# Kernel optimization log

Measured on AMD Instinct MI355X. Metric: run time of the kernel, lower is better.

## Reference

```python
import jax, jax.numpy as jnp
import numpy as np

S, B, D_MODEL, H = 2048, 2, 1024, 16
DH = D_MODEL // H
SCALE = 1.0 / np.sqrt(DH)
NEG_INF = jnp.float32(-1e30)


def setup_inputs() -> dict:
    key = jax.random.key(0)
    ks = jax.random.split(key, 12)
    std = 1.0 / np.sqrt(D_MODEL)
    inp = {
        "query": jax.random.normal(ks[0], (S, B, D_MODEL), jnp.float32),
        "key": jax.random.normal(ks[1], (S, B, D_MODEL), jnp.float32),
        "value": jax.random.normal(ks[2], (S, B, D_MODEL), jnp.float32),
        # causal mask, shape (seq_q, seq_k, 1) per prepare_mask asserts
        "mask": jnp.tril(jnp.ones((S, S), dtype=bool))[:, :, None],
        # params stored (in, out) for x @ W
        "Wq": jax.random.normal(ks[3], (D_MODEL, H * DH), jnp.float32) * std,
        "bq": jnp.zeros((H * DH,), jnp.float32),
        "Wk": jax.random.normal(ks[4], (D_MODEL, H * DH), jnp.float32) * std,
        "bk": jnp.zeros((H * DH,), jnp.float32),
        "Wv": jax.random.normal(ks[5], (D_MODEL, H * DH), jnp.float32) * std,
        "bv": jnp.zeros((H * DH,), jnp.float32),
        "Wo": jax.random.normal(ks[6], (D_MODEL, D_MODEL), jnp.float32) * std,
        "bo": jnp.zeros((D_MODEL,), jnp.float32),
    }
    return inp


def reference(query, key, value, mask, Wq, bq, Wk, bk, Wv, bv, Wo, bo):
    seq_len, batch, _ = query.shape
    # project and split heads: (S, B, H, DH)
    q = (query @ Wq + bq).reshape(seq_len, batch, H, DH)
    k = (key @ Wk + bk).reshape(key.shape[0], batch, H, DH)
    v = (value @ Wv + bv).reshape(value.shape[0], batch, H, DH)
    # scores: (seq_q, batch, heads, seq_k)
    scores = jnp.einsum("ibhd,jbhd->ibhj", q, k) * SCALE
    # mask (seq_q, seq_k, batch_or_1) -> broadcast to (seq_q, batch, 1, seq_k)
    m = jnp.transpose(mask, (0, 2, 1))[:, :, None, :]
    scores = jnp.where(m, scores, NEG_INF)
    attn = jax.nn.softmax(scores, axis=-1)  # dropout_prob=0.0 (eval)
    x = jnp.einsum("ibhj,jbhd->ibhd", attn, v)
    x = x.reshape(seq_len, batch, H * DH)
    return x @ Wo + bo
```

## Files before the change

kernel.cpp:

```cpp
#include <hip/hip_runtime.h>
#include <hip/hip_bf16.h>
#include <cstdint>

#define S_LEN 2048
#define BATCH 2
#define DM    1024
#define NH    16
#define DH    64

typedef short s8v __attribute__((ext_vector_type(8)));
typedef float f4v __attribute__((ext_vector_type(4)));
typedef unsigned int u32x2 __attribute__((ext_vector_type(2)));

__device__ __forceinline__ ushort f2bf(float x) {
  union { float f; uint32_t u; } v; v.f = x;
  uint32_t r = v.u + 0x7fffu + ((v.u >> 16) & 1u);
  return (ushort)(r >> 16);
}
__device__ __forceinline__ float bf2f(ushort u) {
  union { uint32_t u; float f; } v; v.u = (uint32_t)u << 16; return v.f;
}
__device__ __forceinline__ uint32_t fbits(float x) {
  union { float f; uint32_t u; } v; v.f = x; return v.u;
}
__device__ __forceinline__ uint32_t bfrnd(uint32_t u) {
  return u + 0x7fffu + ((u >> 16) & 1u);
}
__device__ __forceinline__ uint32_t packbf(uint32_t flo, uint32_t fhi) {
  return __builtin_amdgcn_perm(bfrnd(fhi), bfrnd(flo), 0x07060302u);
}
__device__ __forceinline__ uint32_t packbf_tr(float lo, float hi) {
  return __builtin_amdgcn_perm(fbits(hi), fbits(lo), 0x07060302u);
}

typedef __attribute__((address_space(1))) const void gas_void;
typedef __attribute__((address_space(3))) void las_void;
__device__ __forceinline__ void gld16(void* l, const void* g) {
  __builtin_amdgcn_global_load_lds((gas_void*)(uintptr_t)g,
                                   (las_void*)(uintptr_t)l, 16, 0, 0);
}

__global__ __launch_bounds__(256)
void prep(const float* W0, const float* W1, const float* W2, const float* W3,
          ushort* T0, ushort* T1, ushort* T2, ushort* T3,
          const float* X0, const float* X1, const float* X2,
          ushort* O0, ushort* O1, ushort* O2) {
  const int z = blockIdx.z;
  if (z < 4) {
    if (blockIdx.x >= 1024) return;
    const float* W = z == 0 ? W0 : z == 1 ? W1 : z == 2 ? W2 : W3;
    ushort*      T = z == 0 ? T0 : z == 1 ? T1 : z == 2 ? T2 : T3;
    __shared__ ushort tile[32][33];
    const int n0 = (blockIdx.x & 31) * 32, k0 = (blockIdx.x >> 5) * 32;
    const int tx = threadIdx.x & 31, ty = threadIdx.x >> 5;
    #pragma unroll
    for (int r = ty; r < 32; r += 8)
      tile[r][tx] = f2bf(W[(size_t)(k0 + r) * DM + n0 + tx]);
    __syncthreads();
    #pragma unroll
    for (int r = ty; r < 32; r += 8)
      T[(size_t)(n0 + r) * DM + k0 + tx] = tile[tx][r];
  } else {
    const float* X = z == 4 ? X0 : z == 5 ? X1 : X2;
    ushort*      O = z == 4 ? O0 : z == 5 ? O1 : O2;
    const size_t i = ((size_t)blockIdx.x * 256 + threadIdx.x) * 4;
    const float4 v = *(const float4*)(X + i);
    ushort4 h;
    h.x = f2bf(v.x); h.y = f2bf(v.y); h.z = f2bf(v.z); h.w = f2bf(v.w);
    *(ushort4*)(O + i) = h;
  }
}

__global__ __launch_bounds__(512, 2)
void gemm_qkv(const ushort* __restrict__ Xq, const ushort* __restrict__ Xk,
              const ushort* __restrict__ Xv,
              const ushort* __restrict__ Wqt, const ushort* __restrict__ Wkt,
              const ushort* __restrict__ Wvt,
              const float* __restrict__ bq, const float* __restrict__ bk,
              const float* __restrict__ bv,
              ushort* __restrict__ Qh, ushort* __restrict__ Kh,
              ushort* __restrict__ Vt) {
  const int z = blockIdx.z;
  const ushort* A    = z == 0 ? Xq  : z == 1 ? Xk  : Xv;
  const ushort* Bt   = z == 0 ? Wqt : z == 1 ? Wkt : Wvt;
  const float*  bias = z == 0 ? bq  : z == 1 ? bk  : bv;

  __shared__ __align__(16) ushort lds[65536];

  const int tid = threadIdx.x, lane = tid & 63, w = tid >> 6;
  const int wm = w >> 2, wn = w & 3;
  const int lrow = lane & 15, quad = lane >> 4;
  const int m0 = blockIdx.x * 256, n0 = blockIdx.y * 256;

  const int tr = tid >> 2;
  const int swz = ((tid & 3) ^ ((tid >> 3) & 3)) * 8;
  const ushort* gA0 = A  + (size_t)(m0 + tr) * DM + swz;
  const ushort* gA1 = A  + (size_t)(m0 + 128 + tr) * DM + swz;
  const ushort* gB0 = Bt + (size_t)(n0 + tr) * DM + swz;
  const ushort* gB1 = Bt + (size_t)(n0 + 128 + tr) * DM + swz;
  const int dA0 = w * 512, dA1 = 4096 + w * 512;
  const int dB0 = 8192 + w * 512, dB1 = 12288 + w * 512;

  const int fr = (lrow >> 1) & 3;
  int pa[8], pb[4];
  #pragma unroll
  for (int i = 0; i < 8; i++)
    pa[i] = (wm * 128 + i * 16 + lrow) * 32 + ((quad ^ fr) * 8);
  #pragma unroll
  for (int j = 0; j < 4; j++)
    pb[j] = 8192 + (wn * 64 + j * 16 + lrow) * 32 + ((quad ^ fr) * 8);

  f4v acc[8][4];
  #pragma unroll
  for (int i = 0; i < 8; i++)
    #pragma unroll
    for (int j = 0; j < 4; j++)
      acc[i][j] = f4v{0.f, 0.f, 0.f, 0.f};

  #pragma unroll
  for (int t = 0; t < 3; t++) {
    const int bb = t * 16384, ko = t * 32;
    gld16(&lds[bb + dA0], gA0 + ko);
    gld16(&lds[bb + dA1], gA1 + ko);
    gld16(&lds[bb + dB0], gB0 + ko);
    gld16(&lds[bb + dB1], gB1 + ko);
  }
  asm volatile("s_waitcnt vmcnt(8)" ::: "memory");
  __builtin_amdgcn_s_barrier();

  for (int t = 0; t < 32; t++) {
    const int bb = (t & 3) * 16384;
    const bool st = t < 29;
    const int sbb = ((t + 3) & 3) * 16384;
    const int ko = (t + 3) * 32;
    s8v af[4], bf[4];
    #pragma unroll
    for (int i = 0; i < 4; i++) af[i] = *(const s8v*)&lds[bb + pa[i]];
    #pragma unroll
    for (int j = 0; j < 4; j++) bf[j] = *(const s8v*)&lds[bb + pb[j]];
    if (st) { gld16(&lds[sbb + dA0], gA0 + ko); gld16(&lds[sbb + dA1], gA1 + ko); }
    __builtin_amdgcn_s_barrier();
    __builtin_amdgcn_s_setprio(1);
    #pragma unroll
    for (int i = 0; i < 4; i++)
      #pragma unroll
      for (int j = 0; j < 4; j++)
        acc[i][j] = __builtin_amdgcn_mfma_f32_16x16x32_bf16(af[i], bf[j], acc[i][j], 0, 0, 0);
    __builtin_amdgcn_s_setprio(0);
    __builtin_amdgcn_s_barrier();
    #pragma unroll
    for (int i = 0; i < 4; i++) af[i] = *(const s8v*)&lds[bb + pa[4 + i]];
    if (st) { gld16(&lds[sbb + dB0], gB0 + ko); gld16(&lds[sbb + dB1], gB1 + ko); }
    __builtin_amdgcn_s_barrier();
    __builtin_amdgcn_s_setprio(1);
    #pragma unroll
    for (int i = 0; i < 4; i++)
      #pragma unroll
      for (int j = 0; j < 4; j++)
        acc[4 + i][j] = __builtin_amdgcn_mfma_f32_16x16x32_bf16(af[i], bf[j], acc[4 + i][j], 0, 0, 0);
    __builtin_amdgcn_s_setprio(0);
    if (t < 29)       asm volatile("s_waitcnt vmcnt(8)" ::: "memory");
    else if (t == 29) asm volatile("s_waitcnt vmcnt(4)" ::: "memory");
    else if (t == 30) asm volatile("s_waitcnt vmcnt(0)" ::: "memory");
    __builtin_amdgcn_s_barrier();
  }

  if (z <= 1) {
    ushort* O = (z == 0) ? Qh : Kh;
    #pragma unroll
    for (int i = 0; i < 8; i++)
      #pragma unroll
      for (int j = 0; j < 4; j++) {
        const int n = n0 + wn * 64 + j * 16 + lrow;
        const float bval = bias[n];
        const int h = n >> 6, d = n & 63;
        const int mb = m0 + wm * 128 + i * 16 + quad * 4;
        #pragma unroll
        for (int r = 0; r < 4; r++) {
          const int m = mb + r;
          O[((size_t)((m & 1) * NH + h) * S_LEN + (m >> 1)) * DH + d] = f2bf(acc[i][j][r] + bval);
        }
      }
  } else {
    ushort* tw = lds + w * 5120;
    const int h = (n0 + wn * 64) >> 6;
    const int s0b = (m0 + wm * 128) >> 1;
    #pragma unroll
    for (int mh = 0; mh < 2; mh++) {
      #pragma unroll
      for (int i = 0; i < 4; i++)
        #pragma unroll
        for (int j = 0; j < 4; j++) {
          const int d_l = j * 16 + lrow;
          const float bval = bias[n0 + wn * 64 + d_l];
          const f4v a = acc[mh * 4 + i][j];
          const int sbase = i * 8 + quad * 2;
          const uint32_t p0 = packbf(fbits(a[0] + bval), fbits(a[2] + bval));
          const uint32_t p1 = packbf(fbits(a[1] + bval), fbits(a[3] + bval));
          *(uint32_t*)&tw[d_l * 40 + sbase]        = p0;
          *(uint32_t*)&tw[2560 + d_l * 40 + sbase] = p1;
        }
      const int s0 = s0b + mh * 32;
      #pragma unroll
      for (int b = 0; b < 2; b++)
        #pragma unroll
        for (int p = 0; p < 4; p++) {
          const int d_l = p * 16 + (lane >> 2);
          const int c   = lane & 3;
          const s8v v = *(const s8v*)&tw[b * 2560 + d_l * 40 + c * 8];
          *(s8v*)&Vt[((size_t)(b * NH + h) * DH + d_l) * S_LEN + s0 + c * 8] = v;
        }
      if (mh == 0) __builtin_amdgcn_s_barrier();
    }
  }
}

__global__ __launch_bounds__(256)
void attn(const ushort* __restrict__ Qh, const ushort* __restrict__ Kh,
          const ushort* __restrict__ Vt, ushort* __restrict__ X,
          ushort* __restrict__ Opart, float* __restrict__ lpart) {
  __shared__ __align__(16) ushort lds[2 * 8192];

  const int tid = threadIdx.x, lane = tid & 63, w = tid >> 6;
  const int lrow = lane & 15, quad = lane >> 4;
  const int bh = blockIdx.x;
  const int slot = blockIdx.y;
  int qt, part, nparts;
  if (slot < 18)      { qt = 15 - slot / 3;        part = slot % 3;        nparts = 3; }
  else if (slot < 30) { qt = 9  - (slot - 18) / 2; part = (slot - 18) % 2; nparts = 2; }
  else                { qt = 33 - slot;            part = 0;               nparts = 1; }
  const int nj  = 2 * qt + 2;
  const int jlo = part * nj / nparts;
  const int jhi = (part + 1) * nj / nparts;
  const int iw  = qt * 128 + w * 32;

  const int srow = lane >> 3;
  const int scol = ((lane & 7) ^ srow) * 8;
  const ushort* gK0 = Kh + ((size_t)bh * S_LEN + 2 * w * 8 + srow) * DH + scol;
  const ushort* gK1 = gK0 + 8 * DH;
  const ushort* gV0 = Vt + ((size_t)bh * DH + 2 * w * 8 + srow) * S_LEN + scol;
  const ushort* gV1 = gV0 + 8 * S_LEN;
  const int lK0 = 2 * w * 512, lK1 = lK0 + 512;
  const int lV0 = 4096 + 2 * w * 512, lV1 = lV0 + 512;

  s8v aq[2][2];
  #pragma unroll
  for (int is = 0; is < 2; is++)
    #pragma unroll
    for (int kk = 0; kk < 2; kk++)
      aq[is][kk] = *(const s8v*)(Qh + ((size_t)bh * S_LEN + iw + is * 16 + lrow) * DH +
                                 kk * 32 + quad * 8);

  const int f8 = lrow & 7;
  int pk[4][2], pv[4][2];
  #pragma unroll
  for (int s4 = 0; s4 < 4; s4++)
    #pragma unroll
    for (int kk = 0; kk < 2; kk++) {
      pk[s4][kk] = (s4 * 16 + lrow) * 64 + (((kk * 4 + quad) ^ f8) * 8);
      pv[s4][kk] = 4096 + (s4 * 16 + lrow) * 64 + (((kk * 4 + quad) ^ f8) * 8);
    }

  f4v o[2][4];
  f4v lacc[2];
  #pragma unroll
  for (int is = 0; is < 2; is++) {
    lacc[is] = f4v{0.f, 0.f, 0.f, 0.f};
    #pragma unroll
    for (int d4 = 0; d4 < 4; d4++) o[is][d4] = f4v{0.f, 0.f, 0.f, 0.f};
  }
  const s8v vones = {0x3F80, 0x3F80, 0x3F80, 0x3F80, 0x3F80, 0x3F80, 0x3F80, 0x3F80};

  {
    const int b0 = (jlo & 1) * 8192;
    const size_t j0 = (size_t)jlo * 64;
    gld16(&lds[b0 + lK0], gK0 + j0 * DH);
    gld16(&lds[b0 + lK1], gK1 + j0 * DH);
    gld16(&lds[b0 + lV0], gV0 + j0);
    gld16(&lds[b0 + lV1], gV1 + j0);
  }

  for (int jt = jlo; jt < jhi; jt++) {
    const int j0 = jt * 64;
    asm volatile("s_waitcnt vmcnt(0)" ::: "memory");
    __builtin_amdgcn_s_barrier();
    const int cur = (jt & 1) * 8192;
    if (jt + 1 < jhi) {
      const int nb = ((jt + 1) & 1) * 8192;
      const size_t jn = (size_t)(jt + 1) * 64;
      gld16(&lds[nb + lK0], gK0 + jn * DH);
      gld16(&lds[nb + lK1], gK1 + jn * DH);
      gld16(&lds[nb + lV0], gV0 + jn);
      gld16(&lds[nb + lV1], gV1 + jn);
    }
    if (j0 > iw + 31) continue;

    f4v sc[2][4];
    #pragma unroll
    for (int is = 0; is < 2; is++)
      #pragma unroll
      for (int s4 = 0; s4 < 4; s4++) sc[is][s4] = f4v{0.f, 0.f, 0.f, 0.f};
    __builtin_amdgcn_s_setprio(1);
    #pragma unroll
    for (int s4 = 0; s4 < 4; s4++) {
      const s8v k0f = *(const s8v*)&lds[cur + pk[s4][0]];
      const s8v k1f = *(const s8v*)&lds[cur + pk[s4][1]];
      sc[0][s4] = __builtin_amdgcn_mfma_f32_16x16x32_bf16(k0f, aq[0][0], sc[0][s4], 0, 0, 0);
      sc[1][s4] = __builtin_amdgcn_mfma_f32_16x16x32_bf16(k0f, aq[1][0], sc[1][s4], 0, 0, 0);
      sc[0][s4] = __builtin_amdgcn_mfma_f32_16x16x32_bf16(k1f, aq[0][1], sc[0][s4], 0, 0, 0);
      sc[1][s4] = __builtin_amdgcn_mfma_f32_16x16x32_bf16(k1f, aq[1][1], sc[1][s4], 0, 0, 0);
    }
    __builtin_amdgcn_s_setprio(0);

    const bool needmask = (j0 + 63) > iw;
    const float C = 0.18033688011112042f;
    uint32_t sw[2][4][2];
    #pragma unroll
    for (int is = 0; is < 2; is++) {
      const int ig = iw + is * 16 + lrow;
      #pragma unroll
      for (int s4 = 0; s4 < 4; s4++) {
        float e0 = __builtin_amdgcn_exp2f(sc[is][s4][0] * C);
        float e1 = __builtin_amdgcn_exp2f(sc[is][s4][1] * C);
        float e2 = __builtin_amdgcn_exp2f(sc[is][s4][2] * C);
        float e3 = __builtin_amdgcn_exp2f(sc[is][s4][3] * C);
        if (needmask) {
          const int jb = j0 + s4 * 16 + quad * 4;
          e0 = (jb + 0 > ig) ? 0.f : e0;
          e1 = (jb + 1 > ig) ? 0.f : e1;
          e2 = (jb + 2 > ig) ? 0.f : e2;
          e3 = (jb + 3 > ig) ? 0.f : e3;
        }
        sw[is][s4][0] = packbf_tr(e0, e1);
        sw[is][s4][1] = packbf_tr(e2, e3);
      }
    }

    s8v ap[2][2];
    #pragma unroll
    for (int is = 0; is < 2; is++)
      #pragma unroll
      for (int kt = 0; kt < 2; kt++) {
        const u32x2 a32 = __builtin_amdgcn_permlane32_swap(
            sw[is][2 * kt][0], sw[is][2 * kt + 1][0], false, false);
        const u32x2 a16 = __builtin_amdgcn_permlane16_swap(a32[0], a32[1], false, false);
        const u32x2 b32 = __builtin_amdgcn_permlane32_swap(
            sw[is][2 * kt][1], sw[is][2 * kt + 1][1], false, false);
        const u32x2 b16 = __builtin_amdgcn_permlane16_swap(b32[0], b32[1], false, false);
        union { uint32_t u[4]; s8v v; } cvt;
        cvt.u[0] = a16[0]; cvt.u[1] = b16[0]; cvt.u[2] = a16[1]; cvt.u[3] = b16[1];
        ap[is][kt] = cvt.v;
      }

    __builtin_amdgcn_s_setprio(1);
    #pragma unroll
    for (int d4 = 0; d4 < 4; d4++) {
      const s8v v0 = *(const s8v*)&lds[cur + pv[d4][0]];
      const s8v v1 = *(const s8v*)&lds[cur + pv[d4][1]];
      o[0][d4] = __builtin_amdgcn_mfma_f32_16x16x32_bf16(ap[0][0], v0, o[0][d4], 0, 0, 0);
      o[1][d4] = __builtin_amdgcn_mfma_f32_16x16x32_bf16(ap[1][0], v0, o[1][d4], 0, 0, 0);
      o[0][d4] = __builtin_amdgcn_mfma_f32_16x16x32_bf16(ap[0][1], v1, o[0][d4], 0, 0, 0);
      o[1][d4] = __builtin_amdgcn_mfma_f32_16x16x32_bf16(ap[1][1], v1, o[1][d4], 0, 0, 0);
    }
    lacc[0] = __builtin_amdgcn_mfma_f32_16x16x32_bf16(ap[0][0], vones, lacc[0], 0, 0, 0);
    lacc[0] = __builtin_amdgcn_mfma_f32_16x16x32_bf16(ap[0][1], vones, lacc[0], 0, 0, 0);
    lacc[1] = __builtin_amdgcn_mfma_f32_16x16x32_bf16(ap[1][0], vones, lacc[1], 0, 0, 0);
    lacc[1] = __builtin_amdgcn_mfma_f32_16x16x32_bf16(ap[1][1], vones, lacc[1], 0, 0, 0);
    __builtin_amdgcn_s_setprio(0);
  }

  if (nparts == 1) {
    const int bb = bh >> 4, h = bh & 15;
    #pragma unroll
    for (int is = 0; is < 2; is++)
      #pragma unroll
      for (int r = 0; r < 4; r++) {
        const float inv = 1.0f / lacc[is][r];
        const int sg = iw + is * 16 + quad * 4 + r;
        #pragma unroll
        for (int d4 = 0; d4 < 4; d4++)
          X[((size_t)sg * BATCH + bb) * DM + h * DH + d4 * 16 + lrow] =
              f2bf(o[is][d4][r] * inv);
      }
  } else {
    ushort* Op = Opart + ((size_t)(bh * 30 + slot) * 128 + w * 32) * 64;
    #pragma unroll
    for (int is = 0; is < 2; is++)
      #pragma unroll
      for (int r = 0; r < 4; r++) {
        const int row_l = is * 16 + quad * 4 + r;
        #pragma unroll
        for (int d4 = 0; d4 < 4; d4++)
          Op[row_l * 64 + d4 * 16 + lrow] = f2bf(o[is][d4][r]);
      }
    if (lrow == 0) {
      float* lp = lpart + (size_t)(bh * 30 + slot) * 128 + w * 32;
      #pragma unroll
      for (int is = 0; is < 2; is++)
        #pragma unroll
        for (int r = 0; r < 4; r++)
          lp[is * 16 + quad * 4 + r] = lacc[is][r];
    }
  }
}

__global__ __launch_bounds__(256)
void combine(const ushort* __restrict__ Opart, const float* __restrict__ lpart,
             ushort* __restrict__ X) {
  const uint32_t gid = blockIdx.x * 256 + threadIdx.x;
  const int dv   = gid & 15;
  const int row  = (gid >> 4) & 127;
  const int rest = gid >> 11;
  const int qi   = rest % 12;
  const int bh   = rest / 12;
  const int qt   = 4 + qi;
  int s0, c;
  if (qt >= 10) { s0 = 3 * (15 - qt); c = 3; }
  else          { s0 = 18 + 2 * (9 - qt); c = 2; }

  float a0 = 0.f, a1 = 0.f, a2 = 0.f, a3 = 0.f, l = 0.f;
  #pragma unroll
  for (int p = 0; p < 3; p++) {
    if (p < c) {
      const size_t base = ((size_t)(bh * 30 + s0 + p) * 128 + row);
      const ushort4 v = *(const ushort4*)&Opart[base * 64 + dv * 4];
      a0 += bf2f(v.x); a1 += bf2f(v.y); a2 += bf2f(v.z); a3 += bf2f(v.w);
      l += lpart[base];
    }
  }
  const float inv = 1.0f / l;
  const int qpos = qt * 128 + row;
  const int b = bh >> 4, h = bh & 15;
  ushort4 hv;
  hv.x = f2bf(a0 * inv);
  hv.y = f2bf(a1 * inv);
  hv.z = f2bf(a2 * inv);
  hv.w = f2bf(a3 * inv);
  *(ushort4*)&X[(((size_t)qpos * BATCH + b) * NH + h) * DH + dv * 4] = hv;
}

__global__ __launch_bounds__(256)
void gemm_out(const ushort* __restrict__ A, const ushort* __restrict__ Bt,
              const float* __restrict__ bias, float* __restrict__ C) {
  __shared__ __align__(16) ushort lds[16384];

  const int tid = threadIdx.x, lane = tid & 63, w = tid >> 6;
  const int wr = w >> 1, wc = w & 1;
  const int lrow = lane & 15, quad = lane >> 4;
  const int m0 = blockIdx.x * 128, n0 = blockIdx.y * 128;

  const int sr4 = lane >> 2;
  const int scol = ((lane & 3) ^ (sr4 & 3)) * 8;

  const ushort* gA[2]; const ushort* gB[2];
  int oA[2], oB[2];
  #pragma unroll
  for (int t = 0; t < 2; t++) {
    const int c = 2 * w + t;
    gA[t] = A  + (size_t)(m0 + c * 16 + sr4) * DM + scol;
    oA[t] = c * 512;
    gB[t] = Bt + (size_t)(n0 + c * 16 + sr4) * DM + scol;
    oB[t] = 4096 + c * 512;
  }

  int pa[4], pb[4];
  #pragma unroll
  for (int i = 0; i < 4; i++) {
    pa[i] = (wr * 64 + i * 16 + lrow) * 32 + ((quad ^ (lrow & 3)) * 8);
    pb[i] = 4096 + (wc * 64 + i * 16 + lrow) * 32 + ((quad ^ (lrow & 3)) * 8);
  }

  f4v acc[4][4];
  #pragma unroll
  for (int i = 0; i < 4; i++)
    #pragma unroll
    for (int j = 0; j < 4; j++)
      acc[i][j] = f4v{0.f, 0.f, 0.f, 0.f};

  #pragma unroll
  for (int t = 0; t < 2; t++) {
    gld16(&lds[oA[t]], gA[t]);
    gld16(&lds[oB[t]], gB[t]);
  }

  for (int ks = 0; ks < 32; ks++) {
    __syncthreads();
    const int bo = (ks & 1) * 8192;
    if (ks < 31) {
      const int nb = ((ks + 1) & 1) * 8192;
      const int ko = (ks + 1) * 32;
      #pragma unroll
      for (int t = 0; t < 2; t++) {
        gld16(&lds[nb + oA[t]], gA[t] + ko);
        gld16(&lds[nb + oB[t]], gB[t] + ko);
      }
    }
    s8v af[4], bf[4];
    #pragma unroll
    for (int i = 0; i < 4; i++) af[i] = *(const s8v*)&lds[bo + pa[i]];
    #pragma unroll
    for (int j = 0; j < 4; j++) bf[j] = *(const s8v*)&lds[bo + pb[j]];
    #pragma unroll
    for (int i = 0; i < 4; i++)
      #pragma unroll
      for (int j = 0; j < 4; j++)
        acc[i][j] = __builtin_amdgcn_mfma_f32_16x16x32_bf16(af[i], bf[j], acc[i][j], 0, 0, 0);
  }

  #pragma unroll
  for (int i = 0; i < 4; i++)
    #pragma unroll
    for (int j = 0; j < 4; j++) {
      const int n = n0 + wc * 64 + j * 16 + lrow;
      const float bval = bias[n];
      const int mb = m0 + wr * 64 + i * 16 + quad * 4;
      #pragma unroll
      for (int r = 0; r < 4; r++)
        C[(size_t)(mb + r) * DM + n] = acc[i][j][r] + bval;
    }
}

extern "C" void kernel_launch(void* const* d_in, const int* in_sizes, int n_in,
                              void* d_out, int out_size, void* d_ws, size_t ws_size,
                              hipStream_t stream) {
  const float* query = (const float*)d_in[0];
  const float* key_  = (const float*)d_in[1];
  const float* value = (const float*)d_in[2];
  const float* Wq = (const float*)d_in[4];
  const float* bq = (const float*)d_in[5];
  const float* Wk = (const float*)d_in[6];
  const float* bk = (const float*)d_in[7];
  const float* Wv = (const float*)d_in[8];
  const float* bv = (const float*)d_in[9];
  const float* Wo = (const float*)d_in[10];
  const float* bo = (const float*)d_in[11];

  ushort* Wqt = (ushort*)d_ws;
  ushort* Wkt = Wqt + (size_t)1024 * 1024;
  ushort* Wvt = Wkt + (size_t)1024 * 1024;
  ushort* Wot = Wvt + (size_t)1024 * 1024;
  ushort* Xbq = Wot + (size_t)1024 * 1024;
  ushort* Xbk = Xbq + (size_t)4 * 1024 * 1024;
  ushort* Xbv = Xbk + (size_t)4 * 1024 * 1024;
  ushort* Qh  = Xbv + (size_t)4 * 1024 * 1024;
  ushort* Kh  = Qh  + (size_t)4 * 1024 * 1024;
  ushort* Vt  = Kh  + (size_t)4 * 1024 * 1024;
  ushort* Opart = Xbk;
  float*  lpart = (float*)Wqt;
  ushort* Xa  = Xbq;

  prep<<<dim3(4096, 1, 7), 256, 0, stream>>>(Wq, Wk, Wv, Wo, Wqt, Wkt, Wvt, Wot,
                                             query, key_, value, Xbq, Xbk, Xbv);
  gemm_qkv<<<dim3(16, 4, 3), 512, 0, stream>>>(Xbq, Xbk, Xbv,
                                               Wqt, Wkt, Wvt, bq, bk, bv,
                                               Qh, Kh, Vt);
  attn<<<dim3(32, 34), 256, 0, stream>>>(Qh, Kh, Vt, Xa, Opart, lpart);
  combine<<<3072, 256, 0, stream>>>(Opart, lpart, Xa);
  gemm_out<<<dim3(32, 8), 256, 0, stream>>>(Xa, Wot, bo, (float*)d_out);
}
```

Baseline: 225.9 us.

## Shrink QKV GEMM tiles, triple-buffer attention K/V, 4-stage pipeline for output GEMM

The QKV projection GEMM moves from 256x256 tiles with 512 threads to 128x128 tiles with 256 threads. This gives 768 blocks instead of 192, so the CUs are better filled. The attention kernel goes from double to triple buffering of K/V tiles, so loads are issued two iterations ahead and the wait only drains the older batch. The output GEMM takes on the same 4-stage async LDS pipeline with split barriers and priority hints that the QKV GEMM uses. Smaller tiles lower data reuse per block, and the extra LDS in attention may reduce occupancy.

```diff
diff --git a/kernel.cpp b/kernel.cpp
--- a/kernel.cpp
+++ b/kernel.cpp
@@ -71,7 +71,7 @@
   }
 }
 
-__global__ __launch_bounds__(512, 2)
+__global__ __launch_bounds__(256, 2)
 void gemm_qkv(const ushort* __restrict__ Xq, const ushort* __restrict__ Xk,
               const ushort* __restrict__ Xv,
               const ushort* __restrict__ Wqt, const ushort* __restrict__ Wkt,
@@ -85,79 +85,80 @@
   const ushort* Bt   = z == 0 ? Wqt : z == 1 ? Wkt : Wvt;
   const float*  bias = z == 0 ? bq  : z == 1 ? bk  : bv;
 
-  __shared__ __align__(16) ushort lds[65536];
+  __shared__ __align__(16) ushort lds[32768];
 
   const int tid = threadIdx.x, lane = tid & 63, w = tid >> 6;
-  const int wm = w >> 2, wn = w & 3;
+  const int wm = w >> 1, wn = w & 1;
   const int lrow = lane & 15, quad = lane >> 4;
-  const int m0 = blockIdx.x * 256, n0 = blockIdx.y * 256;
-
-  const int tr = tid >> 2;
-  const int swz = ((tid & 3) ^ ((tid >> 3) & 3)) * 8;
-  const ushort* gA0 = A  + (size_t)(m0 + tr) * DM + swz;
-  const ushort* gA1 = A  + (size_t)(m0 + 128 + tr) * DM + swz;
-  const ushort* gB0 = Bt + (size_t)(n0 + tr) * DM + swz;
-  const ushort* gB1 = Bt + (size_t)(n0 + 128 + tr) * DM + swz;
-  const int dA0 = w * 512, dA1 = 4096 + w * 512;
-  const int dB0 = 8192 + w * 512, dB1 = 12288 + w * 512;
+  const int m0 = blockIdx.x * 128, n0 = blockIdx.y * 128;
+
+  const int sr4 = lane >> 2;
+  const int scol = ((lane & 3) ^ ((lane >> 3) & 3)) * 8;
+  const ushort* gA[2]; const ushort* gB[2];
+  int dA[2], dB[2];
+  #pragma unroll
+  for (int t = 0; t < 2; t++) {
+    const int c = 2 * w + t;
+    gA[t] = A  + (size_t)(m0 + c * 16 + sr4) * DM + scol;
+    dA[t] = c * 512;
+    gB[t] = Bt + (size_t)(n0 + c * 16 + sr4) * DM + scol;
+    dB[t] = 4096 + c * 512;
+  }
 
   const int fr = (lrow >> 1) & 3;
-  int pa[8], pb[4];
-  #pragma unroll
-  for (int i = 0; i < 8; i++)
-    pa[i] = (wm * 128 + i * 16 + lrow) * 32 + ((quad ^ fr) * 8);
-  #pragma unroll
-  for (int j = 0; j < 4; j++)
-    pb[j] = 8192 + (wn * 64 + j * 16 + lrow) * 32 + ((quad ^ fr) * 8);
-
-  f4v acc[8][4];
-  #pragma unroll
-  for (int i = 0; i < 8; i++)
+  int pa[4], pb[4];
+  #pragma unroll
+  for (int i = 0; i < 4; i++) {
+    pa[i] = (wm * 64 + i * 16 + lrow) * 32 + ((quad ^ fr) * 8);
+    pb[i] = 4096 + (wn * 64 + i * 16 + lrow) * 32 + ((quad ^ fr) * 8);
+  }
+
+  f4v acc[4][4];
+  #pragma unroll
+  for (int i = 0; i < 4; i++)
     #pragma unroll
     for (int j = 0; j < 4; j++)
       acc[i][j] = f4v{0.f, 0.f, 0.f, 0.f};
 
   #pragma unroll
   for (int t = 0; t < 3; t++) {
-    const int bb = t * 16384, ko = t * 32;
-    gld16(&lds[bb + dA0], gA0 + ko);
-    gld16(&lds[bb + dA1], gA1 + ko);
-    gld16(&lds[bb + dB0], gB0 + ko);
-    gld16(&lds[bb + dB1], gB1 + ko);
+    const int bb = t * 8192, ko = t * 32;
+    gld16(&lds[bb + dA[0]], gA[0] + ko);
+    gld16(&lds[bb + dA[1]], gA[1] + ko);
+    gld16(&lds[bb + dB[0]], gB[0] + ko);
+    gld16(&lds[bb + dB[1]], gB[1] + ko);
   }
   asm volatile("s_waitcnt vmcnt(8)" ::: "memory");
   __builtin_amdgcn_s_barrier();
 
   for (int t = 0; t < 32; t++) {
-    const int bb = (t & 3) * 16384;
+    const int bb = (t & 3) * 8192;
     const bool st = t < 29;
-    const int sbb = ((t + 3) & 3) * 16384;
+    const int sbb = ((t + 3) & 3) * 8192;
     const int ko = (t + 3) * 32;
     s8v af[4], bf[4];
     #pragma unroll
     for (int i = 0; i < 4; i++) af[i] = *(const s8v*)&lds[bb + pa[i]];
     #pragma unroll
     for (int j = 0; j < 4; j++) bf[j] = *(const s8v*)&lds[bb + pb[j]];
-    if (st) { gld16(&lds[sbb + dA0], gA0 + ko); gld16(&lds[sbb + dA1], gA1 + ko); }
+    if (st) { gld16(&lds[sbb + dA[0]], gA[0] + ko); gld16(&lds[sbb + dA[1]], gA[1] + ko); }
     __builtin_amdgcn_s_barrier();
     __builtin_amdgcn_s_setprio(1);
     #pragma unroll
-    for (int i = 0; i < 4; i++)
+    for (int i = 0; i < 2; i++)
       #pragma unroll
       for (int j = 0; j < 4; j++)
         acc[i][j] = __builtin_amdgcn_mfma_f32_16x16x32_bf16(af[i], bf[j], acc[i][j], 0, 0, 0);
     __builtin_amdgcn_s_setprio(0);
     __builtin_amdgcn_s_barrier();
-    #pragma unroll
-    for (int i = 0; i < 4; i++) af[i] = *(const s8v*)&lds[bb + pa[4 + i]];
-    if (st) { gld16(&lds[sbb + dB0], gB0 + ko); gld16(&lds[sbb + dB1], gB1 + ko); }
+    if (st) { gld16(&lds[sbb + dB[0]], gB[0] + ko); gld16(&lds[sbb + dB[1]], gB[1] + ko); }
     __builtin_amdgcn_s_barrier();
     __builtin_amdgcn_s_setprio(1);
     #pragma unroll
-    for (int i = 0; i < 4; i++)
+    for (int i = 2; i < 4; i++)
       #pragma unroll
       for (int j = 0; j < 4; j++)
-        acc[4 + i][j] = __builtin_amdgcn_mfma_f32_16x16x32_bf16(af[i], bf[j], acc[4 + i][j], 0, 0, 0);
+        acc[i][j] = __builtin_amdgcn_mfma_f32_16x16x32_bf16(af[i], bf[j], acc[i][j], 0, 0, 0);
     __builtin_amdgcn_s_setprio(0);
     if (t < 29)       asm volatile("s_waitcnt vmcnt(8)" ::: "memory");
     else if (t == 29) asm volatile("s_waitcnt vmcnt(4)" ::: "memory");
@@ -168,13 +169,13 @@
   if (z <= 1) {
     ushort* O = (z == 0) ? Qh : Kh;
     #pragma unroll
-    for (int i = 0; i < 8; i++)
+    for (int i = 0; i < 4; i++)
       #pragma unroll
       for (int j = 0; j < 4; j++) {
         const int n = n0 + wn * 64 + j * 16 + lrow;
         const float bval = bias[n];
         const int h = n >> 6, d = n & 63;
-        const int mb = m0 + wm * 128 + i * 16 + quad * 4;
+        const int mb = m0 + wm * 64 + i * 16 + quad * 4;
         #pragma unroll
         for (int r = 0; r < 4; r++) {
           const int m = mb + r;
@@ -184,34 +185,29 @@
   } else {
     ushort* tw = lds + w * 5120;
     const int h = (n0 + wn * 64) >> 6;
-    const int s0b = (m0 + wm * 128) >> 1;
-    #pragma unroll
-    for (int mh = 0; mh < 2; mh++) {
-      #pragma unroll
-      for (int i = 0; i < 4; i++)
-        #pragma unroll
-        for (int j = 0; j < 4; j++) {
-          const int d_l = j * 16 + lrow;
-          const float bval = bias[n0 + wn * 64 + d_l];
-          const f4v a = acc[mh * 4 + i][j];
-          const int sbase = i * 8 + quad * 2;
-          const uint32_t p0 = packbf(fbits(a[0] + bval), fbits(a[2] + bval));
-          const uint32_t p1 = packbf(fbits(a[1] + bval), fbits(a[3] + bval));
-          *(uint32_t*)&tw[d_l * 40 + sbase]        = p0;
-          *(uint32_t*)&tw[2560 + d_l * 40 + sbase] = p1;
-        }
-      const int s0 = s0b + mh * 32;
-      #pragma unroll
-      for (int b = 0; b < 2; b++)
-        #pragma unroll
-        for (int p = 0; p < 4; p++) {
-          const int d_l = p * 16 + (lane >> 2);
-          const int c   = lane & 3;
-          const s8v v = *(const s8v*)&tw[b * 2560 + d_l * 40 + c * 8];
-          *(s8v*)&Vt[((size_t)(b * NH + h) * DH + d_l) * S_LEN + s0 + c * 8] = v;
-        }
-      if (mh == 0) __builtin_amdgcn_s_barrier();
-    }
+    const int s0 = (m0 + wm * 64) >> 1;
+    #pragma unroll
+    for (int i = 0; i < 4; i++)
+      #pragma unroll
+      for (int j = 0; j < 4; j++) {
+        const int d_l = j * 16 + lrow;
+        const float bval = bias[n0 + wn * 64 + d_l];
+        const f4v a = acc[i][j];
+        const int sbase = i * 8 + quad * 2;
+        const uint32_t p0 = packbf(fbits(a[0] + bval), fbits(a[2] + bval));
+        const uint32_t p1 = packbf(fbits(a[1] + bval), fbits(a[3] + bval));
+        *(uint32_t*)&tw[d_l * 40 + sbase]        = p0;
+        *(uint32_t*)&tw[2560 + d_l * 40 + sbase] = p1;
+      }
+    #pragma unroll
+    for (int b = 0; b < 2; b++)
+      #pragma unroll
+      for (int p = 0; p < 4; p++) {
+        const int d_l = p * 16 + (lane >> 2);
+        const int c   = lane & 3;
+        const s8v v = *(const s8v*)&tw[b * 2560 + d_l * 40 + c * 8];
+        *(s8v*)&Vt[((size_t)(b * NH + h) * DH + d_l) * S_LEN + s0 + c * 8] = v;
+      }
   }
 }
 
@@ -219,7 +215,7 @@
 void attn(const ushort* __restrict__ Qh, const ushort* __restrict__ Kh,
           const ushort* __restrict__ Vt, ushort* __restrict__ X,
           ushort* __restrict__ Opart, float* __restrict__ lpart) {
-  __shared__ __align__(16) ushort lds[2 * 8192];
+  __shared__ __align__(16) ushort lds[3 * 8192];
 
   const int tid = threadIdx.x, lane = tid & 63, w = tid >> 6;
   const int lrow = lane & 15, quad = lane >> 4;
@@ -272,27 +268,38 @@
   const s8v vones = {0x3F80, 0x3F80, 0x3F80, 0x3F80, 0x3F80, 0x3F80, 0x3F80, 0x3F80};
 
   {
-    const int b0 = (jlo & 1) * 8192;
+    const int b0 = (jlo % 3) * 8192;
     const size_t j0 = (size_t)jlo * 64;
     gld16(&lds[b0 + lK0], gK0 + j0 * DH);
     gld16(&lds[b0 + lK1], gK1 + j0 * DH);
     gld16(&lds[b0 + lV0], gV0 + j0);
     gld16(&lds[b0 + lV1], gV1 + j0);
-  }
-
+    if (jlo + 1 < jhi) {
+      const int b1 = ((jlo + 1) % 3) * 8192;
+      const size_t j1 = (size_t)(jlo + 1) * 64;
+      gld16(&lds[b1 + lK0], gK0 + j1 * DH);
+      gld16(&lds[b1 + lK1], gK1 + j1 * DH);
+      gld16(&lds[b1 + lV0], gV0 + j1);
+      gld16(&lds[b1 + lV1], gV1 + j1);
+    }
+  }
+
+  int bcur = jlo % 3;
   for (int jt = jlo; jt < jhi; jt++) {
     const int j0 = jt * 64;
-    asm volatile("s_waitcnt vmcnt(0)" ::: "memory");
-    __builtin_amdgcn_s_barrier();
-    const int cur = (jt & 1) * 8192;
-    if (jt + 1 < jhi) {
-      const int nb = ((jt + 1) & 1) * 8192;
-      const size_t jn = (size_t)(jt + 1) * 64;
-      gld16(&lds[nb + lK0], gK0 + jn * DH);
-      gld16(&lds[nb + lK1], gK1 + jn * DH);
-      gld16(&lds[nb + lV0], gV0 + jn);
-      gld16(&lds[nb + lV1], gV1 + jn);
-    }
+    if (jt + 1 < jhi) asm volatile("s_waitcnt vmcnt(4)" ::: "memory");
+    else              asm volatile("s_waitcnt vmcnt(0)" ::: "memory");
+    __builtin_amdgcn_s_barrier();
+    const int cur = bcur * 8192;
+    if (jt + 2 < jhi) {
+      const int sb = (bcur == 0 ? 2 : bcur - 1) * 8192;
+      const size_t jn = (size_t)(jt + 2) * 64;
+      gld16(&lds[sb + lK0], gK0 + jn * DH);
+      gld16(&lds[sb + lK1], gK1 + jn * DH);
+      gld16(&lds[sb + lV0], gV0 + jn);
+      gld16(&lds[sb + lV1], gV1 + jn);
+    }
+    bcur = (bcur == 2) ? 0 : bcur + 1;
     if (j0 > iw + 31) continue;
 
     f4v sc[2][4];
@@ -439,35 +446,35 @@
   *(ushort4*)&X[(((size_t)qpos * BATCH + b) * NH + h) * DH + dv * 4] = hv;
 }
 
-__global__ __launch_bounds__(256)
+__global__ __launch_bounds__(256, 2)
 void gemm_out(const ushort* __restrict__ A, const ushort* __restrict__ Bt,
               const float* __restrict__ bias, float* __restrict__ C) {
-  __shared__ __align__(16) ushort lds[16384];
+  __shared__ __align__(16) ushort lds[32768];
 
   const int tid = threadIdx.x, lane = tid & 63, w = tid >> 6;
-  const int wr = w >> 1, wc = w & 1;
+  const int wm = w >> 1, wn = w & 1;
   const int lrow = lane & 15, quad = lane >> 4;
   const int m0 = blockIdx.x * 128, n0 = blockIdx.y * 128;
 
   const int sr4 = lane >> 2;
-  const int scol = ((lane & 3) ^ (sr4 & 3)) * 8;
-
+  const int scol = ((lane & 3) ^ ((lane >> 3) & 3)) * 8;
   const ushort* gA[2]; const ushort* gB[2];
-  int oA[2], oB[2];
+  int dA[2], dB[2];
   #pragma unroll
   for (int t = 0; t < 2; t++) {
     const int c = 2 * w + t;
     gA[t] = A  + (size_t)(m0 + c * 16 + sr4) * DM + scol;
-    oA[t] = c * 512;
+    dA[t] = c * 512;
     gB[t] = Bt + (size_t)(n0 + c * 16 + sr4) * DM + scol;
-    oB[t] = 4096 + c * 512;
-  }
-
+    dB[t] = 4096 + c * 512;
+  }
+
+  const int fr = (lrow >> 1) & 3;
   int pa[4], pb[4];
   #pragma unroll
   for (int i = 0; i < 4; i++) {
-    pa[i] = (wr * 64 + i * 16 + lrow) * 32 + ((quad ^ (lrow & 3)) * 8);
-    pb[i] = 4096 + (wc * 64 + i * 16 + lrow) * 32 + ((quad ^ (lrow & 3)) * 8);
+    pa[i] = (wm * 64 + i * 16 + lrow) * 32 + ((quad ^ fr) * 8);
+    pb[i] = 4096 + (wn * 64 + i * 16 + lrow) * 32 + ((quad ^ fr) * 8);
   }
 
   f4v acc[4][4];
@@ -478,42 +485,58 @@
       acc[i][j] = f4v{0.f, 0.f, 0.f, 0.f};
 
   #pragma unroll
-  for (int t = 0; t < 2; t++) {
-    gld16(&lds[oA[t]], gA[t]);
-    gld16(&lds[oB[t]], gB[t]);
-  }
-
-  for (int ks = 0; ks < 32; ks++) {
-    __syncthreads();
-    const int bo = (ks & 1) * 8192;
-    if (ks < 31) {
-      const int nb = ((ks + 1) & 1) * 8192;
-      const int ko = (ks + 1) * 32;
-      #pragma unroll
-      for (int t = 0; t < 2; t++) {
-        gld16(&lds[nb + oA[t]], gA[t] + ko);
-        gld16(&lds[nb + oB[t]], gB[t] + ko);
-      }
-    }
+  for (int t = 0; t < 3; t++) {
+    const int bb = t * 8192, ko = t * 32;
+    gld16(&lds[bb + dA[0]], gA[0] + ko);
+    gld16(&lds[bb + dA[1]], gA[1] + ko);
+    gld16(&lds[bb + dB[0]], gB[0] + ko);
+    gld16(&lds[bb + dB[1]], gB[1] + ko);
+  }
+  asm volatile("s_waitcnt vmcnt(8)" ::: "memory");
+  __builtin_amdgcn_s_barrier();
+
+  for (int t = 0; t < 32; t++) {
+    const int bb = (t & 3) * 8192;
+    const bool st = t < 29;
+    const int sbb = ((t + 3) & 3) * 8192;
+    const int ko = (t + 3) * 32;
     s8v af[4], bf[4];
     #pragma unroll
-    for (int i = 0; i < 4; i++) af[i] = *(const s8v*)&lds[bo + pa[i]];
-    #pragma unroll
-    for (int j = 0; j < 4; j++) bf[j] = *(const s8v*)&lds[bo + pb[j]];
-    #pragma unroll
-    for (int i = 0; i < 4; i++)
+    for (int i = 0; i < 4; i++) af[i] = *(const s8v*)&lds[bb + pa[i]];
+    #pragma unroll
+    for (int j = 0; j < 4; j++) bf[j] = *(const s8v*)&lds[bb + pb[j]];
+    if (st) { gld16(&lds[sbb + dA[0]], gA[0] + ko); gld16(&lds[sbb + dA[1]], gA[1] + ko); }
+    __builtin_amdgcn_s_barrier();
+    __builtin_amdgcn_s_setprio(1);
+    #pragma unroll
+    for (int i = 0; i < 2; i++)
       #pragma unroll
       for (int j = 0; j < 4; j++)
         acc[i][j] = __builtin_amdgcn_mfma_f32_16x16x32_bf16(af[i], bf[j], acc[i][j], 0, 0, 0);
+    __builtin_amdgcn_s_setprio(0);
+    __builtin_amdgcn_s_barrier();
+    if (st) { gld16(&lds[sbb + dB[0]], gB[0] + ko); gld16(&lds[sbb + dB[1]], gB[1] + ko); }
+    __builtin_amdgcn_s_barrier();
+    __builtin_amdgcn_s_setprio(1);
+    #pragma unroll
+    for (int i = 2; i < 4; i++)
+      #pragma unroll
+      for (int j = 0; j < 4; j++)
+        acc[i][j] = __builtin_amdgcn_mfma_f32_16x16x32_bf16(af[i], bf[j], acc[i][j], 0, 0, 0);
+    __builtin_amdgcn_s_setprio(0);
+    if (t < 29)       asm volatile("s_waitcnt vmcnt(8)" ::: "memory");
+    else if (t == 29) asm volatile("s_waitcnt vmcnt(4)" ::: "memory");
+    else if (t == 30) asm volatile("s_waitcnt vmcnt(0)" ::: "memory");
+    __builtin_amdgcn_s_barrier();
   }
 
   #pragma unroll
   for (int i = 0; i < 4; i++)
     #pragma unroll
     for (int j = 0; j < 4; j++) {
-      const int n = n0 + wc * 64 + j * 16 + lrow;
+      const int n = n0 + wn * 64 + j * 16 + lrow;
       const float bval = bias[n];
-      const int mb = m0 + wr * 64 + i * 16 + quad * 4;
+      const int mb = m0 + wm * 64 + i * 16 + quad * 4;
       #pragma unroll
       for (int r = 0; r < 4; r++)
         C[(size_t)(mb + r) * DM + n] = acc[i][j][r] + bval;
@@ -551,7 +574,7 @@
 
   prep<<<dim3(4096, 1, 7), 256, 0, stream>>>(Wq, Wk, Wv, Wo, Wqt, Wkt, Wvt, Wot,
                                              query, key_, value, Xbq, Xbk, Xbv);
-  gemm_qkv<<<dim3(16, 4, 3), 512, 0, stream>>>(Xbq, Xbk, Xbv,
+  gemm_qkv<<<dim3(32, 8, 3), 256, 0, stream>>>(Xbq, Xbk, Xbv,
                                                Wqt, Wkt, Wvt, bq, bk, bv,
                                                Qh, Kh, Vt);
   attn<<<dim3(32, 34), 256, 0, stream>>>(Qh, Kh, Vt, Xa, Opart, lpart);
```

Measured after the change: 223.1 us. Within noise of the previous version (-1.2%).
